# Optimization experiments

Hardware: AMD Instinct MI355X
Metric: run time of the kernel (lower is better)

The kernel has to match this reference:

```python
import jax, jax.numpy as jnp
import numpy as np

N_USERS = 100000
N_ITEMS = 50000
D = 64
IMG_D = 1024
TXT_D = 384
N_EDGES = 2000000
GNN_LAYERS = 2
CAT_RATE = 0.55
NORM_SCALE = 1.0


def setup_inputs() -> dict:
    key = jax.random.key(0)
    ks = jax.random.split(key, 12)
    return {
        "image_feats": jax.random.normal(ks[0], (N_ITEMS, IMG_D), jnp.float32),
        "text_feats": jax.random.normal(ks[1], (N_ITEMS, TXT_D), jnp.float32),
        "user_emb": jax.random.normal(ks[2], (N_USERS, D), jnp.float32) * 0.1,
        "item_emb": jax.random.normal(ks[3], (N_ITEMS, D), jnp.float32) * 0.1,
        "W_img": jax.random.normal(ks[4], (IMG_D, D), jnp.float32) / np.sqrt(IMG_D),
        "b_img": jnp.zeros((D,), jnp.float32),
        "W_txt": jax.random.normal(ks[5], (TXT_D, D), jnp.float32) / np.sqrt(TXT_D),
        "b_txt": jnp.zeros((D,), jnp.float32),
        "val_ui": jax.random.uniform(ks[6], (N_EDGES,), jnp.float32) * 0.05,
        "val_iu": jax.random.uniform(ks[7], (N_EDGES,), jnp.float32) * 0.05,
        "edge_u": jax.random.randint(ks[8], (N_EDGES,), 0, N_USERS, jnp.int32),
        "edge_i": jax.random.randint(ks[9], (N_EDGES,), 0, N_ITEMS, jnp.int32),
    }


def _l2norm(x, eps=1e-12):
    # F.normalize(x, p=2, dim=1)
    n = jnp.maximum(jnp.linalg.norm(x, axis=1, keepdims=True), eps)
    return x / n


def reference(image_feats, text_feats, user_emb, item_emb,
              W_img, b_img, W_txt, b_txt, val_ui, val_iu, edge_u, edge_i):
    def spmm_ui(X):  # ui_graph @ X : [n_items, d] -> [n_users, d]
        return jax.ops.segment_sum(val_ui[:, None] * X[edge_i], edge_u,
                                   num_segments=N_USERS)

    def spmm_iu(X):  # iu_graph @ X : [n_users, d] -> [n_items, d]
        return jax.ops.segment_sum(val_iu[:, None] * X[edge_u], edge_i,
                                   num_segments=N_ITEMS)

    # prompt_module is None -> prompt_user/prompt_item are zeros, so the
    # feat_prompt terms (normalize of zeros) vanish. Dropout in eval = identity.
    image_feat = image_feats @ W_img + b_img  # [n_items, D]
    text_feat = text_feats @ W_txt + b_txt    # [n_items, D]

    # The original loop recomputes identical values every iteration (image_feat
    # is never updated), so one pass gives the same result.
    image_user = spmm_ui(image_feat)
    image_item = spmm_iu(image_user)
    text_user = spmm_ui(text_feat)
    text_item = spmm_iu(text_user)

    # soft_token_rate * normalize(zeros) == 0 -> id embeddings unchanged
    combined = jnp.concatenate([user_emb, item_emb], axis=0)
    # NormLayer mode 'PN' (PairNorm): center, then scale by mean row norm
    c = combined - combined.mean(axis=0, keepdims=True)
    rownorm_mean = jnp.sqrt(jnp.mean(jnp.sum(c * c, axis=1)) + 1e-6)
    normed = NORM_SCALE * c / rownorm_mean
    u_g, i_g = normed[:N_USERS], normed[N_USERS:]

    u_acc, i_acc = u_g, i_g
    for _ in range(GNN_LAYERS):  # is_softmax=False branch
        u_g = spmm_ui(i_g)
        i_g = spmm_iu(u_g)
        u_acc = u_acc + u_g
        i_acc = i_acc + i_g
    user_embeddings = u_acc / (GNN_LAYERS + 1)
    item_embeddings = i_acc / (GNN_LAYERS + 1)

    u_out = (user_embeddings + CAT_RATE * _l2norm(image_user)
             + CAT_RATE * _l2norm(text_user))
    i_out = (item_embeddings + CAT_RATE * _l2norm(image_item)
             + CAT_RATE * _l2norm(text_item))
    return (u_out, i_out, image_item, text_item, image_user, text_user)
```

## Files before the change

kernel.cpp:

```cpp
#include <hip/hip_runtime.h>
#include <cstdint>
#include <cstddef>

#define N_USERS 100000
#define N_ITEMS 50000
#define DIM     64
#define IMG_D   1024
#define TXT_D   384
#define N_EDGES 2000000
#define N_COMB  (N_USERS + N_ITEMS)

#define OFF_UOUT 0
#define OFF_IOUT (N_USERS * DIM)
#define OFF_IIT  (OFF_IOUT + N_ITEMS * DIM)
#define OFF_TIT  (OFF_IIT + N_ITEMS * DIM)
#define OFF_IUS  (OFF_TIT + N_ITEMS * DIM)
#define OFF_TUS  (OFF_IUS + N_USERS * DIM)

typedef __attribute__((ext_vector_type(8))) short short8;
typedef __attribute__((ext_vector_type(4))) float float4v;
typedef __attribute__((ext_vector_type(4))) unsigned int uint4v;
typedef __attribute__((ext_vector_type(4))) _Float16 half4v;

__device__ __forceinline__ float wave_sum64(float v) {
#pragma unroll
  for (int off = 32; off; off >>= 1) v += __shfl_xor(v, off, 64);
  return v;
}

__device__ __forceinline__ unsigned int pack_bf16(float x, float y) {
  const unsigned int xu = __float_as_uint(x) + 0x8000u;
  const unsigned int yu = __float_as_uint(y) + 0x8000u;
  return (xu >> 16) | (yu & 0xffff0000u);
}

__device__ __forceinline__ float4v fma4h(float w, const half4v x, float4v a) {
#pragma unroll
  for (int j = 0; j < 4; ++j) a[j] = fmaf(w, (float)x[j], a[j]);
  return a;
}

__device__ __forceinline__ half4v to_h4(const float4v a) {
  half4v h;
#pragma unroll
  for (int j = 0; j < 4; ++j) h[j] = (_Float16)a[j];
  return h;
}

__device__ __forceinline__ void dec_rec(unsigned int rec, int& c, float& w) {
  c = (int)(rec >> 15);
  w = (float)__builtin_bit_cast(_Float16, (unsigned short)(rec & 0x7FFFu));
}

__device__ __forceinline__ unsigned int enc_rec(int c, float w) {
  const unsigned short hb = __builtin_bit_cast(unsigned short, (_Float16)w);
  return ((unsigned int)c << 15) | (unsigned int)hb;
}

__global__ __launch_bounds__(256) void hist_kernel(const int* __restrict__ eu,
                                                   const int* __restrict__ ei,
                                                   int* __restrict__ cu, int* __restrict__ ci,
                                                   int* __restrict__ pe_u, int* __restrict__ pe_i) {
  const int i = blockIdx.x * 256 + threadIdx.x;
  if (i < N_EDGES) {
    pe_u[i] = atomicAdd(&cu[eu[i]], 1);
    pe_i[i] = atomicAdd(&ci[ei[i]], 1);
  }
}

__global__ __launch_bounds__(1024) void scan2_kernel(const int* __restrict__ cnt_u,
                                                     int* __restrict__ rs_u,
                                                     const int* __restrict__ cnt_i,
                                                     int* __restrict__ rs_i) {
  const int* counts;
  int *rs, n;
  if (blockIdx.x == 0) { counts = cnt_u; rs = rs_u; n = N_USERS; }
  else                 { counts = cnt_i; rs = rs_i; n = N_ITEMS; }
  __shared__ int part[1024];
  const int t = threadIdx.x;
  const int chunk = (n + 1023) >> 10;
  const int b = t * chunk;
  const int e = min(b + chunk, n);
  int s = 0;
  for (int j = b; j < e; ++j) s += counts[j];
  part[t] = s;
  __syncthreads();
  for (int off = 1; off < 1024; off <<= 1) {
    const int add = (t >= off) ? part[t - off] : 0;
    __syncthreads();
    part[t] += add;
    __syncthreads();
  }
  int run = (t == 0) ? 0 : part[t - 1];
  for (int j = b; j < e; ++j) {
    rs[j] = run;
    run += counts[j];
  }
  if (t == 1023) rs[n] = part[1023];
}

__global__ __launch_bounds__(256) void fill_kernel(
    const int* __restrict__ eu, const int* __restrict__ ei,
    const float* __restrict__ vui, const float* __restrict__ viu,
    const int* __restrict__ pe_u, const int* __restrict__ pe_i,
    const int* __restrict__ rs_u, const int* __restrict__ rs_i,
    unsigned int* __restrict__ cw_u, unsigned int* __restrict__ cw_i) {
  const int i = blockIdx.x * 256 + threadIdx.x;
  if (i < N_EDGES) {
    const int u = eu[i], it = ei[i];
    const int p = rs_u[u] + pe_u[i];
    const int q = rs_i[it] + pe_i[i];
    cw_u[p] = enc_rec(it, vui[i]);
    cw_i[q] = enc_rec(u, viu[i]);
  }
}

__global__ __launch_bounds__(256) void wswizzle_kernel(const float* __restrict__ Wimg,
                                                       const float* __restrict__ Wtxt,
                                                       unsigned short* __restrict__ WBimg,
                                                       unsigned short* __restrict__ WBtxt) {
  int t = blockIdx.x * 256 + threadIdx.x;
  const float* W;
  unsigned short* WB;
  if (t < 8192) { W = Wimg; WB = WBimg; }
  else if (t < 8192 + 3072) { t -= 8192; W = Wtxt; WB = WBtxt; }
  else return;
  const int frag = t >> 6;
  const int lane = t & 63;
  const int K0idx = frag >> 2;
  const int n0idx = frag & 3;
  const int k0 = K0idx * 32 + ((lane >> 4) << 3);
  const int c = n0idx * 16 + (lane & 15);
  unsigned short us[8];
#pragma unroll
  for (int j = 0; j < 8; ++j) {
    const unsigned int b = __float_as_uint(W[(size_t)(k0 + j) * 64 + c]) + 0x8000u;
    us[j] = (unsigned short)(b >> 16);
  }
  uint4v o;
  o.x = (unsigned int)us[0] | ((unsigned int)us[1] << 16);
  o.y = (unsigned int)us[2] | ((unsigned int)us[3] << 16);
  o.z = (unsigned int)us[4] | ((unsigned int)us[5] << 16);
  o.w = (unsigned int)us[6] | ((unsigned int)us[7] << 16);
  *reinterpret_cast<uint4v*>(WB + (size_t)t * 8) = o;
}

__global__ __launch_bounds__(256) void mfma_gemm_kernel(
    const float* __restrict__ Ximg, const unsigned short* __restrict__ WBimg,
    const float* __restrict__ bimg,
    const float* __restrict__ Xtxt, const unsigned short* __restrict__ WBtxt,
    const float* __restrict__ btxt,
    _Float16* __restrict__ g_items) {
  const int TILES_IMG = N_ITEMS / 16;
  const int wv = threadIdx.x >> 6;
  const int lane = threadIdx.x & 63;
  int tile = blockIdx.x * 4 + wv;
  if (tile >= 2 * TILES_IMG) return;

  const float* X;
  const unsigned short* WB;
  const float* bias;
  int K, nK0, c0;
  if (tile < TILES_IMG) { X = Ximg; WB = WBimg; bias = bimg; K = IMG_D; nK0 = IMG_D / 32; c0 = 0; }
  else { tile -= TILES_IMG; X = Xtxt; WB = WBtxt; bias = btxt; K = TXT_D; nK0 = TXT_D / 32; c0 = 64; }

  const int row0 = tile * 16;
  const int m = lane & 15;
  const int koff = (lane >> 4) << 3;
  const float* __restrict__ xp = X + (size_t)(row0 + m) * K + koff;
  const short8* __restrict__ wb8 = reinterpret_cast<const short8*>(WB);

  float4v acc[4];
#pragma unroll
  for (int n0 = 0; n0 < 4; ++n0) acc[n0] = (float4v){0.f, 0.f, 0.f, 0.f};

  for (int K0 = 0; K0 < nK0; ++K0) {
    const float4 xa = *reinterpret_cast<const float4*>(xp + K0 * 32);
    const float4 xb = *reinterpret_cast<const float4*>(xp + K0 * 32 + 4);
    uint4v au;
    au.x = pack_bf16(xa.x, xa.y);
    au.y = pack_bf16(xa.z, xa.w);
    au.z = pack_bf16(xb.x, xb.y);
    au.w = pack_bf16(xb.z, xb.w);
    const short8 af = __builtin_bit_cast(short8, au);
#pragma unroll
    for (int n0 = 0; n0 < 4; ++n0) {
      const short8 bf = wb8[(size_t)(K0 * 4 + n0) * 64 + lane];
      acc[n0] = __builtin_amdgcn_mfma_f32_16x16x32_bf16(af, bf, acc[n0], 0, 0, 0);
    }
  }

  const int crow = (lane >> 4) << 2;
  const int ccol = lane & 15;
#pragma unroll
  for (int n0 = 0; n0 < 4; ++n0) {
    const float bv = bias[n0 * 16 + ccol];
#pragma unroll
    for (int r = 0; r < 4; ++r) {
      g_items[(size_t)(row0 + crow + r) * 192 + c0 + n0 * 16 + ccol] =
          (_Float16)(acc[n0][r] + bv);
    }
  }
}

__global__ __launch_bounds__(256) void stats_kernel(const float* __restrict__ ue,
                                                    const float* __restrict__ ie,
                                                    float* __restrict__ stats) {
  const int t = threadIdx.x;
  const int lane = t & 63;
  float cs = 0.f, ss = 0.f;
  const size_t total = (size_t)N_COMB * DIM;
  const size_t ubound = (size_t)N_USERS * DIM;
  const size_t stride = (size_t)gridDim.x * blockDim.x;
  for (size_t i = (size_t)blockIdx.x * blockDim.x + t; i < total; i += stride) {
    const float v = (i < ubound) ? ue[i] : ie[i - ubound];
    cs += v;
    ss += v * v;
  }
  ss = wave_sum64(ss);
  __shared__ float lcol[4][64];
  __shared__ float lss[4];
  const int wv = t >> 6;
  lcol[wv][lane] = cs;
  if (lane == 0) lss[wv] = ss;
  __syncthreads();
  if (wv == 0) {
    const float c = lcol[0][lane] + lcol[1][lane] + lcol[2][lane] + lcol[3][lane];
    atomicAdd(&stats[lane], c);
    if (lane == 0) atomicAdd(&stats[64], lss[0] + lss[1] + lss[2] + lss[3]);
  }
}

__global__ void finalize_kernel(float* __restrict__ stats) {
  const int d = threadIdx.x;
  const float ssum = stats[64];
  const float m = stats[d] / (float)N_COMB;
  const float m2sum = wave_sum64(m * m);
  const float tot = ssum - (float)N_COMB * m2sum;
  const float rnm = sqrtf(tot / (float)N_COMB + 1e-6f);
  stats[d] = m;
  if (d == 0) stats[64] = 1.f / rnm;
}

__global__ __launch_bounds__(256) void normalize_kernel(
    const float* __restrict__ ue, const float* __restrict__ ie, const float* __restrict__ stats,
    float* __restrict__ uacc, float* __restrict__ iacc, _Float16* __restrict__ g_items) {
  const int lane = threadIdx.x & 63;
  const float m = stats[lane];
  const float inv = stats[64];
  const size_t total = (size_t)N_COMB * DIM;
  const size_t ubound = (size_t)N_USERS * DIM;
  const size_t stride = (size_t)gridDim.x * blockDim.x;
  for (size_t i = (size_t)blockIdx.x * blockDim.x + threadIdx.x; i < total; i += stride) {
    if (i < ubound) {
      uacc[i] = (ue[i] - m) * inv;
    } else {
      const size_t j = i - ubound;
      const float v = (ie[j] - m) * inv;
      iacc[j] = v;
      g_items[(j >> 6) * 192 + 128 + (j & 63)] = (_Float16)v;
    }
  }
}

__global__ __launch_bounds__(256) void spmm_triple_kernel(
    const int* __restrict__ rs, const unsigned int* __restrict__ cw,
    const _Float16* __restrict__ G,
    float* __restrict__ O1, float* __restrict__ O2,
    float* __restrict__ acc,
    _Float16* __restrict__ gout192, _Float16* __restrict__ gout64, int nrows) {
  const int lane = threadIdx.x & 63;
  const int wv = __builtin_amdgcn_readfirstlane(threadIdx.x >> 6);
  const int r = blockIdx.x * 4 + wv;
  if (r >= nrows) return;
  const int q = lane >> 4;
  const int l = lane & 15;
  const int s = rs[r], e = rs[r + 1];
  float4v a1 = {0.f, 0.f, 0.f, 0.f};
  float4v a2 = {0.f, 0.f, 0.f, 0.f};
  float4v a3 = {0.f, 0.f, 0.f, 0.f};
  int k = s + q;
  for (; k + 4 < e; k += 8) {
    int c0, c1;
    float w0, w1;
    dec_rec(cw[k], c0, w0);
    dec_rec(cw[k + 4], c1, w1);
    const _Float16* g0 = G + (size_t)c0 * 192 + l * 4;
    const _Float16* g1 = G + (size_t)c1 * 192 + l * 4;
    const half4v x10 = *reinterpret_cast<const half4v*>(g0);
    const half4v x20 = *reinterpret_cast<const half4v*>(g0 + 64);
    const half4v x30 = *reinterpret_cast<const half4v*>(g0 + 128);
    const half4v x11 = *reinterpret_cast<const half4v*>(g1);
    const half4v x21 = *reinterpret_cast<const half4v*>(g1 + 64);
    const half4v x31 = *reinterpret_cast<const half4v*>(g1 + 128);
    a1 = fma4h(w0, x10, a1);
    a2 = fma4h(w0, x20, a2);
    a3 = fma4h(w0, x30, a3);
    a1 = fma4h(w1, x11, a1);
    a2 = fma4h(w1, x21, a2);
    a3 = fma4h(w1, x31, a3);
  }
  if (k < e) {
    int c0;
    float w0;
    dec_rec(cw[k], c0, w0);
    const _Float16* g0 = G + (size_t)c0 * 192 + l * 4;
    a1 = fma4h(w0, *reinterpret_cast<const half4v*>(g0), a1);
    a2 = fma4h(w0, *reinterpret_cast<const half4v*>(g0 + 64), a2);
    a3 = fma4h(w0, *reinterpret_cast<const half4v*>(g0 + 128), a3);
  }
#pragma unroll
  for (int j = 0; j < 4; ++j) {
    a1[j] += __shfl_xor(a1[j], 16, 64);
    a1[j] += __shfl_xor(a1[j], 32, 64);
    a2[j] += __shfl_xor(a2[j], 16, 64);
    a2[j] += __shfl_xor(a2[j], 32, 64);
    a3[j] += __shfl_xor(a3[j], 16, 64);
    a3[j] += __shfl_xor(a3[j], 32, 64);
  }
  if (q == 0) {
    const size_t o = (size_t)r * 64 + l * 4;
    *reinterpret_cast<float4v*>(O1 + o) = a1;
    *reinterpret_cast<float4v*>(O2 + o) = a2;
    float4v av = *reinterpret_cast<const float4v*>(acc + o);
#pragma unroll
    for (int j = 0; j < 4; ++j) av[j] += a3[j];
    *reinterpret_cast<float4v*>(acc + o) = av;
    if (gout192) {
      _Float16* gr = gout192 + (size_t)r * 192 + l * 4;
      *reinterpret_cast<half4v*>(gr) = to_h4(a1);
      *reinterpret_cast<half4v*>(gr + 64) = to_h4(a2);
      *reinterpret_cast<half4v*>(gr + 128) = to_h4(a3);
    } else {
      *reinterpret_cast<half4v*>(gout64 + o) = to_h4(a3);
    }
  }
}

__global__ __launch_bounds__(256) void spmm_final_kernel(
    const int* __restrict__ rs, const unsigned int* __restrict__ cw,
    const _Float16* __restrict__ X, _Float16* __restrict__ GO,
    const float* __restrict__ P, const float* __restrict__ Q,
    float* __restrict__ accio, int nrows) {
  const int lane = threadIdx.x & 63;
  const int wv = __builtin_amdgcn_readfirstlane(threadIdx.x >> 6);
  const int r = blockIdx.x * 4 + wv;
  if (r >= nrows) return;
  const int q = lane >> 4;
  const int l = lane & 15;
  const int s = rs[r], e = rs[r + 1];
  float4v a = {0.f, 0.f, 0.f, 0.f};
  int k = s + q;
  for (; k + 4 < e; k += 8) {
    int c0, c1;
    float w0, w1;
    dec_rec(cw[k], c0, w0);
    dec_rec(cw[k + 4], c1, w1);
    const half4v x0 = *reinterpret_cast<const half4v*>(X + (size_t)c0 * 64 + l * 4);
    const half4v x1 = *reinterpret_cast<const half4v*>(X + (size_t)c1 * 64 + l * 4);
    a = fma4h(w0, x0, a);
    a = fma4h(w1, x1, a);
  }
  if (k < e) {
    int c0;
    float w0;
    dec_rec(cw[k], c0, w0);
    a = fma4h(w0, *reinterpret_cast<const half4v*>(X + (size_t)c0 * 64 + l * 4), a);
  }
#pragma unroll
  for (int j = 0; j < 4; ++j) {
    a[j] += __shfl_xor(a[j], 16, 64);
    a[j] += __shfl_xor(a[j], 32, 64);
  }
  const size_t o = (size_t)r * 64 + l * 4;
  const float4v p = *reinterpret_cast<const float4v*>(P + o);
  const float4v qv = *reinterpret_cast<const float4v*>(Q + o);
  float ps = p[0] * p[0] + p[1] * p[1] + p[2] * p[2] + p[3] * p[3];
  float qs = qv[0] * qv[0] + qv[1] * qv[1] + qv[2] * qv[2] + qv[3] * qv[3];
#pragma unroll
  for (int off = 8; off; off >>= 1) {
    ps += __shfl_xor(ps, off, 64);
    qs += __shfl_xor(qs, off, 64);
  }
  const float pn = 0.55f / fmaxf(sqrtf(ps), 1e-12f);
  const float qn = 0.55f / fmaxf(sqrtf(qs), 1e-12f);
  if (q == 0) {
    if (GO) *reinterpret_cast<half4v*>(GO + o) = to_h4(a);
    float4v av = *reinterpret_cast<const float4v*>(accio + o);
#pragma unroll
    for (int j = 0; j < 4; ++j) {
      av[j] = (av[j] + a[j]) * (1.0f / 3.0f) + pn * p[j] + qn * qv[j];
    }
    *reinterpret_cast<float4v*>(accio + o) = av;
  }
}

extern "C" void kernel_launch(void* const* d_in, const int* in_sizes, int n_in,
                              void* d_out, int out_size, void* d_ws, size_t ws_size,
                              hipStream_t stream) {
  const float* image_feats = (const float*)d_in[0];
  const float* text_feats = (const float*)d_in[1];
  const float* user_emb = (const float*)d_in[2];
  const float* item_emb = (const float*)d_in[3];
  const float* W_img = (const float*)d_in[4];
  const float* b_img = (const float*)d_in[5];
  const float* W_txt = (const float*)d_in[6];
  const float* b_txt = (const float*)d_in[7];
  const float* val_ui = (const float*)d_in[8];
  const float* val_iu = (const float*)d_in[9];
  const int* edge_u = (const int*)d_in[10];
  const int* edge_i = (const int*)d_in[11];

  float* out = (float*)d_out;
  float* u_acc = out + OFF_UOUT;
  float* i_acc = out + OFF_IOUT;
  float* img_item = out + OFF_IIT;
  float* txt_item = out + OFF_TIT;
  float* img_user = out + OFF_IUS;
  float* txt_user = out + OFF_TUS;

  char* wsb = (char*)d_ws;
  size_t off = 0;
  auto take = [&](size_t bytes) -> void* {
    void* p = wsb + off;
    off += (bytes + 255) & ~(size_t)255;
    return p;
  };
  _Float16* g_items = (_Float16*)take((size_t)N_ITEMS * 192 * 2);
  _Float16* g_users = (_Float16*)take((size_t)N_USERS * 192 * 2);
  _Float16* g_i1 = (_Float16*)take((size_t)N_ITEMS * 64 * 2);
  _Float16* g_u2 = (_Float16*)take((size_t)N_USERS * 64 * 2);
  unsigned int* cw_u = (unsigned int*)take((size_t)N_EDGES * 4);
  unsigned int* cw_i = (unsigned int*)take((size_t)N_EDGES * 4);
  int* rs_u = (int*)take((N_USERS + 1) * 4);
  int* rs_i = (int*)take((N_ITEMS + 1) * 4);
  int* cnt_u = (int*)take((size_t)N_USERS * 4);
  int* cnt_i = (int*)take((size_t)N_ITEMS * 4);
  unsigned short* WBimg = (unsigned short*)take((size_t)8192 * 8 * 2);
  unsigned short* WBtxt = (unsigned short*)take((size_t)3072 * 8 * 2);
  float* stats = (float*)take(65 * 4);

  int* pe_u = (int*)g_users;
  int* pe_i = pe_u + N_EDGES;

  hipMemsetAsync(cnt_u, 0, (size_t)N_USERS * 4, stream);
  hipMemsetAsync(cnt_i, 0, (size_t)N_ITEMS * 4, stream);
  hipMemsetAsync(stats, 0, 65 * 4, stream);

  const int eblk = (N_EDGES + 255) / 256;
  hist_kernel<<<eblk, 256, 0, stream>>>(edge_u, edge_i, cnt_u, cnt_i, pe_u, pe_i);
  scan2_kernel<<<2, 1024, 0, stream>>>(cnt_u, rs_u, cnt_i, rs_i);
  fill_kernel<<<eblk, 256, 0, stream>>>(edge_u, edge_i, val_ui, val_iu, pe_u, pe_i,
                                        rs_u, rs_i, cw_u, cw_i);

  wswizzle_kernel<<<44, 256, 0, stream>>>(W_img, W_txt, WBimg, WBtxt);
  const int ntiles = 2 * (N_ITEMS / 16);
  mfma_gemm_kernel<<<(ntiles + 3) / 4, 256, 0, stream>>>(image_feats, WBimg, b_img,
                                                         text_feats, WBtxt, b_txt, g_items);

  stats_kernel<<<2048, 256, 0, stream>>>(user_emb, item_emb, stats);
  finalize_kernel<<<1, 64, 0, stream>>>(stats);
  normalize_kernel<<<2048, 256, 0, stream>>>(user_emb, item_emb, stats, u_acc, i_acc, g_items);

  spmm_triple_kernel<<<N_USERS / 4, 256, 0, stream>>>(
      rs_u, cw_u, g_items, img_user, txt_user, u_acc, g_users, nullptr, N_USERS);
  spmm_triple_kernel<<<N_ITEMS / 4, 256, 0, stream>>>(
      rs_i, cw_i, g_users, img_item, txt_item, i_acc, nullptr, g_i1, N_ITEMS);
  spmm_final_kernel<<<N_USERS / 4, 256, 0, stream>>>(
      rs_u, cw_u, g_i1, g_u2, img_user, txt_user, u_acc, N_USERS);
  spmm_final_kernel<<<N_ITEMS / 4, 256, 0, stream>>>(
      rs_i, cw_i, g_u2, nullptr, img_item, txt_item, i_acc, N_ITEMS);
}
```

Measured before the change: 1.248 ms.

## Privatize CSR histogram per block to cut global atomic contention

Replaces the single global-atomic histogram with 64 per-block private count arrays, each built over a contiguous edge chunk using workgroup-scoped atomics. Added kernels sum the private counts for the scan, then convert each private array into per-block base offsets that the fill kernel uses. This aims to reduce contention and coherence cost on the global atomic counters. In exchange it needs a large memset (64×150k ints) and strided reductions, and the histogram runs on only 64 blocks, which limits parallelism.

```diff
diff --git a/kernel.cpp b/kernel.cpp
--- a/kernel.cpp
+++ b/kernel.cpp
@@ -10,6 +10,9 @@
 #define N_EDGES 2000000
 #define N_COMB  (N_USERS + N_ITEMS)
 
+#define NPRIV  64
+#define ECHUNK ((N_EDGES + NPRIV - 1) / NPRIV)
+
 #define OFF_UOUT 0
 #define OFF_IOUT (N_USERS * DIM)
 #define OFF_IIT  (OFF_IOUT + N_ITEMS * DIM)
@@ -57,14 +60,39 @@
   return ((unsigned int)c << 15) | (unsigned int)hb;
 }
 
-__global__ __launch_bounds__(256) void hist_kernel(const int* __restrict__ eu,
-                                                   const int* __restrict__ ei,
-                                                   int* __restrict__ cu, int* __restrict__ ci,
-                                                   int* __restrict__ pe_u, int* __restrict__ pe_i) {
-  const int i = blockIdx.x * 256 + threadIdx.x;
-  if (i < N_EDGES) {
-    pe_u[i] = atomicAdd(&cu[eu[i]], 1);
-    pe_i[i] = atomicAdd(&ci[ei[i]], 1);
+__global__ __launch_bounds__(256) void hist_priv_kernel(
+    const int* __restrict__ eu, const int* __restrict__ ei,
+    int* __restrict__ priv_u, int* __restrict__ priv_i,
+    int* __restrict__ pe_u, int* __restrict__ pe_i) {
+  const int b = blockIdx.x;
+  int* __restrict__ pu = priv_u + (size_t)b * N_USERS;
+  int* __restrict__ pi = priv_i + (size_t)b * N_ITEMS;
+  const int s = b * ECHUNK;
+  const int e = min(s + ECHUNK, N_EDGES);
+  for (int i = s + (int)threadIdx.x; i < e; i += 256) {
+    const int u = eu[i], it = ei[i];
+    pe_u[i] = __hip_atomic_fetch_add(&pu[u], 1, __ATOMIC_RELAXED,
+                                     __HIP_MEMORY_SCOPE_WORKGROUP);
+    pe_i[i] = __hip_atomic_fetch_add(&pi[it], 1, __ATOMIC_RELAXED,
+                                     __HIP_MEMORY_SCOPE_WORKGROUP);
+  }
+}
+
+__global__ __launch_bounds__(256) void sum_priv_kernel(
+    const int* __restrict__ priv_u, const int* __restrict__ priv_i,
+    int* __restrict__ cnt_u, int* __restrict__ cnt_i) {
+  const int t = blockIdx.x * 256 + threadIdx.x;
+  if (t < N_USERS) {
+    int ssum = 0;
+#pragma unroll 4
+    for (int b = 0; b < NPRIV; ++b) ssum += priv_u[(size_t)b * N_USERS + t];
+    cnt_u[t] = ssum;
+  } else if (t < N_USERS + N_ITEMS) {
+    const int k = t - N_USERS;
+    int ssum = 0;
+#pragma unroll 4
+    for (int b = 0; b < NPRIV; ++b) ssum += priv_i[(size_t)b * N_ITEMS + k];
+    cnt_i[k] = ssum;
   }
 }
 
@@ -99,17 +127,42 @@
   if (t == 1023) rs[n] = part[1023];
 }
 
+__global__ __launch_bounds__(256) void base_priv_kernel(
+    int* __restrict__ priv_u, int* __restrict__ priv_i,
+    const int* __restrict__ rs_u, const int* __restrict__ rs_i) {
+  const int t = blockIdx.x * 256 + threadIdx.x;
+  if (t < N_USERS) {
+    int run = rs_u[t];
+    for (int b = 0; b < NPRIV; ++b) {
+      const size_t idx = (size_t)b * N_USERS + t;
+      const int c = priv_u[idx];
+      priv_u[idx] = run;
+      run += c;
+    }
+  } else if (t < N_USERS + N_ITEMS) {
+    const int k = t - N_USERS;
+    int run = rs_i[k];
+    for (int b = 0; b < NPRIV; ++b) {
+      const size_t idx = (size_t)b * N_ITEMS + k;
+      const int c = priv_i[idx];
+      priv_i[idx] = run;
+      run += c;
+    }
+  }
+}
+
 __global__ __launch_bounds__(256) void fill_kernel(
     const int* __restrict__ eu, const int* __restrict__ ei,
     const float* __restrict__ vui, const float* __restrict__ viu,
     const int* __restrict__ pe_u, const int* __restrict__ pe_i,
-    const int* __restrict__ rs_u, const int* __restrict__ rs_i,
+    const int* __restrict__ priv_u, const int* __restrict__ priv_i,
     unsigned int* __restrict__ cw_u, unsigned int* __restrict__ cw_i) {
   const int i = blockIdx.x * 256 + threadIdx.x;
   if (i < N_EDGES) {
+    const int b = i / ECHUNK;
     const int u = eu[i], it = ei[i];
-    const int p = rs_u[u] + pe_u[i];
-    const int q = rs_i[it] + pe_i[i];
+    const int p = priv_u[(size_t)b * N_USERS + u] + pe_u[i];
+    const int q = priv_i[(size_t)b * N_ITEMS + it] + pe_i[i];
     cw_u[p] = enc_rec(it, vui[i]);
     cw_i[q] = enc_rec(u, viu[i]);
   }
@@ -440,18 +493,22 @@
   unsigned short* WBtxt = (unsigned short*)take((size_t)3072 * 8 * 2);
   float* stats = (float*)take(65 * 4);
 
-  int* pe_u = (int*)g_users;
+  int* priv_u = (int*)g_users;
+  int* priv_i = (int*)((char*)g_users + (size_t)NPRIV * N_USERS * 4);
+  int* pe_u = (int*)g_i1;
   int* pe_i = pe_u + N_EDGES;
 
-  hipMemsetAsync(cnt_u, 0, (size_t)N_USERS * 4, stream);
-  hipMemsetAsync(cnt_i, 0, (size_t)N_ITEMS * 4, stream);
+  hipMemsetAsync(priv_u, 0, (size_t)NPRIV * (N_USERS + N_ITEMS) * 4, stream);
   hipMemsetAsync(stats, 0, 65 * 4, stream);
 
+  hist_priv_kernel<<<NPRIV, 256, 0, stream>>>(edge_u, edge_i, priv_u, priv_i, pe_u, pe_i);
+  const int kblk = (N_USERS + N_ITEMS + 255) / 256;
+  sum_priv_kernel<<<kblk, 256, 0, stream>>>(priv_u, priv_i, cnt_u, cnt_i);
+  scan2_kernel<<<2, 1024, 0, stream>>>(cnt_u, rs_u, cnt_i, rs_i);
+  base_priv_kernel<<<kblk, 256, 0, stream>>>(priv_u, priv_i, rs_u, rs_i);
   const int eblk = (N_EDGES + 255) / 256;
-  hist_kernel<<<eblk, 256, 0, stream>>>(edge_u, edge_i, cnt_u, cnt_i, pe_u, pe_i);
-  scan2_kernel<<<2, 1024, 0, stream>>>(cnt_u, rs_u, cnt_i, rs_i);
   fill_kernel<<<eblk, 256, 0, stream>>>(edge_u, edge_i, val_ui, val_iu, pe_u, pe_i,
-                                        rs_u, rs_i, cw_u, cw_i);
+                                        priv_u, priv_i, cw_u, cw_i);
 
   wswizzle_kernel<<<44, 256, 0, stream>>>(W_img, W_txt, WBimg, WBtxt);
   const int ntiles = 2 * (N_ITEMS / 16);
```

New measurement: 1.335 ms. 1.07x slower.
